# Performance work log

Hardware: AMD Instinct MI355X
Metric: run time of the kernel (lower is better)

The kernel has to match this reference:

```python
import jax, jax.numpy as jnp
import numpy as np

DIM = 1024
HEADS = 8
DIM_HEAD = 64
DIM_INNER = HEADS * DIM_HEAD  # 512


def setup_inputs() -> dict:
    key = jax.random.key(0)
    k1, k2, k3, k4 = jax.random.split(key, 4)
    x = jax.random.normal(k1, (1, 4096, DIM), dtype=jnp.float32)
    gamma = jnp.ones((DIM,), dtype=jnp.float32)
    w_qkv = jax.random.normal(k2, (DIM, 3 * DIM_INNER), dtype=jnp.float32) * (DIM ** -0.5)
    w_out = jax.random.normal(k3, (DIM_INNER, DIM), dtype=jnp.float32) * (DIM_INNER ** -0.5)
    return {"x": x, "gamma": gamma, "w_qkv": w_qkv, "w_out": w_out}


def _rmsnorm(x, gamma):
    # F.normalize(x, dim=-1) * sqrt(dim) * gamma
    norm = jnp.sqrt(jnp.sum(x * x, axis=-1, keepdims=True))
    x = x / jnp.maximum(norm, 1e-12)
    return x * (DIM ** 0.5) * gamma


def reference(x, gamma, w_qkv, w_out):
    b, n, _ = x.shape
    h, d = HEADS, DIM_HEAD
    normed = _rmsnorm(x, gamma)
    qkv = normed @ w_qkv  # [b, n, 3*h*d]
    qkv = qkv.reshape(b, n, 3, h, d)
    q = jnp.transpose(qkv[:, :, 0], (0, 2, 1, 3))  # b h n d
    k = jnp.transpose(qkv[:, :, 1], (0, 2, 1, 3))
    v = jnp.transpose(qkv[:, :, 2], (0, 2, 1, 3))
    # default_attention (faithful: scales q by d**0.5 as in source)
    q = q * (d ** 0.5)
    sim = jnp.einsum('bhid,bhjd->bhij', q, k)
    mask_value = -jnp.finfo(sim.dtype).max
    causal_mask = jnp.triu(jnp.ones((n, n), dtype=bool), 1)
    sim = jnp.where(causal_mask, mask_value, sim)
    attn = jax.nn.softmax(sim, axis=-1)
    out = jnp.einsum('bhij,bhjd->bhid', attn, v)  # b h n d
    out = jnp.transpose(out, (0, 2, 1, 3)).reshape(b, n, h * d)
    return out @ w_out  # [b, n, dim]
```

## Files before the change

kernel.cpp:

```cpp
#include <hip/hip_runtime.h>
#include <math.h>

#define SEQ 4096
#define DIM 1024
#define HEADS 8
#define DINNER 512
#define QKVW 1536
#define PAD 80

typedef unsigned short u16;
typedef __attribute__((ext_vector_type(8))) short s8v;
typedef __attribute__((ext_vector_type(4))) float f4v;
#define MFMA(a, b, c) __builtin_amdgcn_mfma_f32_16x16x32_bf16(a, b, c, 0, 0, 0)

__device__ __forceinline__ u16 f2bf(float f) {
    unsigned u = __float_as_uint(f);
    u += 0x7fff + ((u >> 16) & 1);
    return (u16)(u >> 16);
}
__device__ __forceinline__ float bf2f(u16 b) { return __uint_as_float(((unsigned)b) << 16); }

__global__ __launch_bounds__(256) void rmsnorm_split(const float* __restrict__ x,
                                                     const float* __restrict__ gamma,
                                                     u16* __restrict__ hi,
                                                     u16* __restrict__ lo) {
    __shared__ float red[4];
    const int row = blockIdx.x, t = threadIdx.x;
    const float* xr = x + (size_t)row * DIM;
    float v[4];
    float ss = 0.f;
#pragma unroll
    for (int i = 0; i < 4; ++i) { v[i] = xr[t + i * 256]; ss += v[i] * v[i]; }
#pragma unroll
    for (int off = 32; off >= 1; off >>= 1) ss += __shfl_xor(ss, off, 64);
    if ((t & 63) == 0) red[t >> 6] = ss;
    __syncthreads();
    float scale = 32.0f / fmaxf(sqrtf(red[0] + red[1] + red[2] + red[3]), 1e-12f);
#pragma unroll
    for (int i = 0; i < 4; ++i) {
        int c = t + i * 256;
        float y = v[i] * scale * gamma[c];
        u16 h = f2bf(y);
        hi[(size_t)row * DIM + c] = h;
        lo[(size_t)row * DIM + c] = f2bf(y - bf2f(h));
    }
}

__global__ __launch_bounds__(256) void transpose_split(const float* __restrict__ in,
                                                       u16* __restrict__ hi,
                                                       u16* __restrict__ lo,
                                                       int R, int C, int want_lo) {
    __shared__ float tile[64][65];
    const int c0 = blockIdx.x * 64, r0 = blockIdx.y * 64;
    const int t = threadIdx.x, col = t & 63, rb = t >> 6;
#pragma unroll
    for (int j = 0; j < 16; ++j)
        tile[rb + j * 4][col] = in[(size_t)(r0 + rb + j * 4) * C + c0 + col];
    __syncthreads();
#pragma unroll
    for (int j = 0; j < 16; ++j) {
        int cc = rb + j * 4;
        float v = tile[col][cc];
        size_t oi = (size_t)(c0 + cc) * R + r0 + col;
        u16 h = f2bf(v);
        hi[oi] = h;
        if (want_lo) lo[oi] = f2bf(v - bf2f(h));
    }
}

__global__ __launch_bounds__(256) void gemm_qkv_split(
    const u16* __restrict__ Ah, const u16* __restrict__ Al,
    const u16* __restrict__ Bh, const u16* __restrict__ Bl,
    u16* __restrict__ qh, u16* __restrict__ ql,
    u16* __restrict__ kh, u16* __restrict__ kl, u16* __restrict__ vtp) {
    __shared__ u16 Ash[64 * PAD], Asl[64 * PAD], Bsh[64 * PAD], Bsl[64 * PAD];
    const int t = threadIdx.x;
    const int bn = blockIdx.x * 64, bm = blockIdx.y * 64;
    const int w = t >> 6, lane = t & 63, m = lane & 15, q = lane >> 4;
    f4v acc[4] = {{0.f, 0.f, 0.f, 0.f}, {0.f, 0.f, 0.f, 0.f},
                  {0.f, 0.f, 0.f, 0.f}, {0.f, 0.f, 0.f, 0.f}};
    for (int k0 = 0; k0 < DIM; k0 += 64) {
        __syncthreads();
#pragma unroll
        for (int i = 0; i < 2; ++i) {
            int c = t + i * 256, row = c >> 3, ch = (c & 7) * 8;
            *(uint4*)&Ash[row * PAD + ch] = *(const uint4*)&Ah[(size_t)(bm + row) * DIM + k0 + ch];
            *(uint4*)&Asl[row * PAD + ch] = *(const uint4*)&Al[(size_t)(bm + row) * DIM + k0 + ch];
            *(uint4*)&Bsh[row * PAD + ch] = *(const uint4*)&Bh[(size_t)(bn + row) * DIM + k0 + ch];
            *(uint4*)&Bsl[row * PAD + ch] = *(const uint4*)&Bl[(size_t)(bn + row) * DIM + k0 + ch];
        }
        __syncthreads();
#pragma unroll
        for (int kk = 0; kk < 64; kk += 32) {
            s8v ah = *(const s8v*)&Ash[(w * 16 + m) * PAD + kk + q * 8];
            s8v al = *(const s8v*)&Asl[(w * 16 + m) * PAD + kk + q * 8];
#pragma unroll
            for (int ct = 0; ct < 4; ++ct) {
                s8v bh = *(const s8v*)&Bsh[(ct * 16 + m) * PAD + kk + q * 8];
                s8v bl = *(const s8v*)&Bsl[(ct * 16 + m) * PAD + kk + q * 8];
                acc[ct] = MFMA(ah, bh, acc[ct]);
                acc[ct] = MFMA(al, bh, acc[ct]);
                acc[ct] = MFMA(ah, bl, acc[ct]);
            }
        }
    }
    const int region = bn >> 9;
#pragma unroll
    for (int ct = 0; ct < 4; ++ct) {
#pragma unroll
        for (int r = 0; r < 4; ++r) {
            int gr = bm + w * 16 + q * 4 + r;
            int gc = bn + ct * 16 + m;
            float v = acc[ct][r];
            if (region == 0) {
                v *= 8.0f;
                u16 h = f2bf(v);
                qh[(size_t)gr * DINNER + gc] = h;
                ql[(size_t)gr * DINNER + gc] = f2bf(v - bf2f(h));
            } else if (region == 1) {
                u16 h = f2bf(v);
                kh[(size_t)gr * DINNER + (gc - 512)] = h;
                kl[(size_t)gr * DINNER + (gc - 512)] = f2bf(v - bf2f(h));
            } else {
                vtp[(size_t)(gc - 1024) * SEQ + gr] = f2bf(v);
            }
        }
    }
}

__global__ __launch_bounds__(256) void attn_mfma(
    const u16* __restrict__ qh, const u16* __restrict__ ql,
    const u16* __restrict__ kh, const u16* __restrict__ kl,
    const u16* __restrict__ vt, u16* __restrict__ atto) {
    __shared__ u16 Qh[64 * PAD], Ql[64 * PAD], KP[64 * PAD], Kl[64 * PAD], Vt[64 * PAD];
    const int t = threadIdx.x;
    const int qt = blockIdx.x, h = blockIdx.y;
    const int w = t >> 6, lane = t & 63, m = lane & 15, q = lane >> 4;

#pragma unroll
    for (int i = 0; i < 2; ++i) {
        int c = t + i * 256, row = c >> 3, ch = (c & 7) * 8;
        *(uint4*)&Qh[row * PAD + ch] =
            *(const uint4*)&qh[(size_t)(qt * 64 + row) * DINNER + h * 64 + ch];
        *(uint4*)&Ql[row * PAD + ch] =
            *(const uint4*)&ql[(size_t)(qt * 64 + row) * DINNER + h * 64 + ch];
    }

    f4v o[4] = {{0.f, 0.f, 0.f, 0.f}, {0.f, 0.f, 0.f, 0.f},
                {0.f, 0.f, 0.f, 0.f}, {0.f, 0.f, 0.f, 0.f}};
    float mi[4] = {-1e30f, -1e30f, -1e30f, -1e30f};
    float li[4] = {0.f, 0.f, 0.f, 0.f};

    for (int kt = 0; kt <= qt; ++kt) {
        __syncthreads();
#pragma unroll
        for (int i = 0; i < 2; ++i) {
            int c = t + i * 256, row = c >> 3, ch = (c & 7) * 8;
            *(uint4*)&KP[row * PAD + ch] =
                *(const uint4*)&kh[(size_t)(kt * 64 + row) * DINNER + h * 64 + ch];
            *(uint4*)&Kl[row * PAD + ch] =
                *(const uint4*)&kl[(size_t)(kt * 64 + row) * DINNER + h * 64 + ch];
            *(uint4*)&Vt[row * PAD + ch] =
                *(const uint4*)&vt[(size_t)(h * 64 + row) * SEQ + kt * 64 + ch];
        }
        __syncthreads();

        f4v s[4] = {{0.f, 0.f, 0.f, 0.f}, {0.f, 0.f, 0.f, 0.f},
                    {0.f, 0.f, 0.f, 0.f}, {0.f, 0.f, 0.f, 0.f}};
#pragma unroll
        for (int kk = 0; kk < 64; kk += 32) {
            s8v ah = *(const s8v*)&Qh[(w * 16 + m) * PAD + kk + q * 8];
            s8v al = *(const s8v*)&Ql[(w * 16 + m) * PAD + kk + q * 8];
#pragma unroll
            for (int ct = 0; ct < 4; ++ct) {
                s8v bh = *(const s8v*)&KP[(ct * 16 + m) * PAD + kk + q * 8];
                s8v bl = *(const s8v*)&Kl[(ct * 16 + m) * PAD + kk + q * 8];
                s[ct] = MFMA(ah, bh, s[ct]);
                s[ct] = MFMA(al, bh, s[ct]);
                s[ct] = MFMA(ah, bl, s[ct]);
            }
        }
        if (kt == qt) {
#pragma unroll
            for (int ct = 0; ct < 4; ++ct)
#pragma unroll
                for (int r = 0; r < 4; ++r)
                    if (ct * 16 + m > w * 16 + q * 4 + r) s[ct][r] = -1e30f;
        }

        float alpha[4];
#pragma unroll
        for (int r = 0; r < 4; ++r) {
            float rm = fmaxf(fmaxf(s[0][r], s[1][r]), fmaxf(s[2][r], s[3][r]));
#pragma unroll
            for (int off = 8; off >= 1; off >>= 1) rm = fmaxf(rm, __shfl_xor(rm, off, 64));
            float mn = fmaxf(mi[r], rm);
            alpha[r] = __expf(mi[r] - mn);
            mi[r] = mn;
            float rs = 0.f;
#pragma unroll
            for (int ct = 0; ct < 4; ++ct) {
                s[ct][r] = __expf(s[ct][r] - mn);
                rs += s[ct][r];
            }
#pragma unroll
            for (int off = 8; off >= 1; off >>= 1) rs += __shfl_xor(rs, off, 64);
            li[r] = li[r] * alpha[r] + rs;
        }

        __syncthreads();
#pragma unroll
        for (int ct = 0; ct < 4; ++ct)
#pragma unroll
            for (int r = 0; r < 4; ++r) {
                KP[(w * 16 + q * 4 + r) * PAD + ct * 16 + m] = f2bf(s[ct][r]);
                o[ct][r] *= alpha[r];
            }
#pragma unroll
        for (int kk = 0; kk < 64; kk += 32) {
            s8v ap = *(const s8v*)&KP[(w * 16 + m) * PAD + kk + q * 8];
#pragma unroll
            for (int ct = 0; ct < 4; ++ct) {
                s8v bv = *(const s8v*)&Vt[(ct * 16 + m) * PAD + kk + q * 8];
                o[ct] = MFMA(ap, bv, o[ct]);
            }
        }
    }

#pragma unroll
    for (int r = 0; r < 4; ++r) {
        float inv = 1.0f / li[r];
#pragma unroll
        for (int ct = 0; ct < 4; ++ct)
            atto[(size_t)(qt * 64 + w * 16 + q * 4 + r) * DINNER + h * 64 + ct * 16 + m] =
                f2bf(o[ct][r] * inv);
    }
}

__global__ __launch_bounds__(256) void gemm_out_bf16(const u16* __restrict__ A,
                                                     const u16* __restrict__ Bt,
                                                     float* __restrict__ C) {
    __shared__ u16 As[64 * PAD], Bs[64 * PAD];
    const int t = threadIdx.x;
    const int bn = blockIdx.x * 64, bm = blockIdx.y * 64;
    const int w = t >> 6, lane = t & 63, m = lane & 15, q = lane >> 4;
    f4v acc[4] = {{0.f, 0.f, 0.f, 0.f}, {0.f, 0.f, 0.f, 0.f},
                  {0.f, 0.f, 0.f, 0.f}, {0.f, 0.f, 0.f, 0.f}};
    for (int k0 = 0; k0 < DINNER; k0 += 64) {
        __syncthreads();
#pragma unroll
        for (int i = 0; i < 2; ++i) {
            int c = t + i * 256, row = c >> 3, ch = (c & 7) * 8;
            *(uint4*)&As[row * PAD + ch] = *(const uint4*)&A[(size_t)(bm + row) * DINNER + k0 + ch];
            *(uint4*)&Bs[row * PAD + ch] = *(const uint4*)&Bt[(size_t)(bn + row) * DINNER + k0 + ch];
        }
        __syncthreads();
#pragma unroll
        for (int kk = 0; kk < 64; kk += 32) {
            s8v a = *(const s8v*)&As[(w * 16 + m) * PAD + kk + q * 8];
#pragma unroll
            for (int ct = 0; ct < 4; ++ct) {
                s8v b = *(const s8v*)&Bs[(ct * 16 + m) * PAD + kk + q * 8];
                acc[ct] = MFMA(a, b, acc[ct]);
            }
        }
    }
#pragma unroll
    for (int ct = 0; ct < 4; ++ct)
#pragma unroll
        for (int r = 0; r < 4; ++r)
            C[(size_t)(bm + w * 16 + q * 4 + r) * DIM + bn + ct * 16 + m] = acc[ct][r];
}

extern "C" void kernel_launch(void* const* d_in, const int* in_sizes, int n_in,
                              void* d_out, int out_size, void* d_ws, size_t ws_size,
                              hipStream_t stream) {
    const float* x     = (const float*)d_in[0];
    const float* gamma = (const float*)d_in[1];
    const float* w_qkv = (const float*)d_in[2];
    const float* w_out = (const float*)d_in[3];
    float* out = (float*)d_out;

    u16* nh = (u16*)d_out;
    u16* nl = nh + (size_t)SEQ * DIM;

    u16* p = (u16*)d_ws;
    u16* wqt_h = p; p += (size_t)QKVW * DIM;
    u16* wqt_l = p; p += (size_t)QKVW * DIM;
    u16* wot   = p; p += (size_t)DIM * DINNER;
    u16* qh = p; p += (size_t)SEQ * DINNER;
    u16* ql = p; p += (size_t)SEQ * DINNER;
    u16* kh = p; p += (size_t)SEQ * DINNER;
    u16* kl = p; p += (size_t)SEQ * DINNER;
    u16* vt = p; p += (size_t)DINNER * SEQ;
    u16* atto = p; p += (size_t)SEQ * DINNER;

    transpose_split<<<dim3(QKVW / 64, DIM / 64), 256, 0, stream>>>(w_qkv, wqt_h, wqt_l,
                                                                   DIM, QKVW, 1);
    transpose_split<<<dim3(DIM / 64, DINNER / 64), 256, 0, stream>>>(w_out, wot, nullptr,
                                                                     DINNER, DIM, 0);
    rmsnorm_split<<<SEQ, 256, 0, stream>>>(x, gamma, nh, nl);
    gemm_qkv_split<<<dim3(QKVW / 64, SEQ / 64), 256, 0, stream>>>(nh, nl, wqt_h, wqt_l,
                                                                  qh, ql, kh, kl, vt);
    attn_mfma<<<dim3(SEQ / 64, HEADS), 256, 0, stream>>>(qh, ql, kh, kl, vt, atto);
    gemm_out_bf16<<<dim3(DIM / 64, SEQ / 64), 256, 0, stream>>>(atto, wot, out);
}
```

Before: 299.3 us.

## Split causal attention across key chunks with a separate merge kernel

Replaces the single per-query-tile attention kernel with a split-KV version. The keys are divided into chunks of 16 tiles, each block produces partial outputs plus per-row max and sum, and a merge kernel combines them into the attention output. The split kernel also loads Q straight into registers and prefetches the next K/V tile in registers. The goal is to fix the poor load balance and low parallelism of causal attention, where long query rows ran serially. In exchange it adds partial-output traffic (reusing the output buffer and workspace), an extra launch and a merge pass, and it falls back to the old kernel if the workspace is too small.

```diff
diff --git a/kernel.cpp b/kernel.cpp
--- a/kernel.cpp
+++ b/kernel.cpp
@@ -7,6 +7,7 @@
 #define DINNER 512
 #define QKVW 1536
 #define PAD 80
+#define CHUNK 16
 
 typedef unsigned short u16;
 typedef __attribute__((ext_vector_type(8))) short s8v;
@@ -128,6 +129,171 @@
     }
 }
 
+__global__ __launch_bounds__(256, 4) void attn_chunk(
+    const u16* __restrict__ qhp, const u16* __restrict__ qlp,
+    const u16* __restrict__ kh, const u16* __restrict__ kl,
+    const u16* __restrict__ vt,
+    float* __restrict__ po0, float* __restrict__ po1,
+    float* __restrict__ po2, float* __restrict__ po3,
+    float* __restrict__ ml) {
+    __shared__ u16 KP[64 * PAD], Kl[64 * PAD], Vt[64 * PAD];
+    const int t = threadIdx.x;
+    const int bx = blockIdx.x;
+    const int qt = 63 - (bx >> 2), c = bx & 3, h = blockIdx.y;
+    if (c * CHUNK > qt) return;
+    const int kt0 = c * CHUNK;
+    const int kt1 = (qt < kt0 + CHUNK - 1) ? qt : (kt0 + CHUNK - 1);
+    const int w = t >> 6, lane = t & 63, m = lane & 15, q = lane >> 4;
+
+    const size_t qrow = (size_t)(qt * 64 + w * 16 + m) * DINNER + h * 64;
+    const s8v qf_h0 = *(const s8v*)&qhp[qrow + q * 8];
+    const s8v qf_h1 = *(const s8v*)&qhp[qrow + 32 + q * 8];
+    const s8v qf_l0 = *(const s8v*)&qlp[qrow + q * 8];
+    const s8v qf_l1 = *(const s8v*)&qlp[qrow + 32 + q * 8];
+
+    f4v o[4] = {{0.f, 0.f, 0.f, 0.f}, {0.f, 0.f, 0.f, 0.f},
+                {0.f, 0.f, 0.f, 0.f}, {0.f, 0.f, 0.f, 0.f}};
+    float mi[4] = {-1e30f, -1e30f, -1e30f, -1e30f};
+    float li[4] = {0.f, 0.f, 0.f, 0.f};
+
+    uint4 rk[2], rl[2], rv[2];
+#pragma unroll
+    for (int i = 0; i < 2; ++i) {
+        int c2 = t + i * 256, row = c2 >> 3, ch = (c2 & 7) * 8;
+        rk[i] = *(const uint4*)&kh[(size_t)(kt0 * 64 + row) * DINNER + h * 64 + ch];
+        rl[i] = *(const uint4*)&kl[(size_t)(kt0 * 64 + row) * DINNER + h * 64 + ch];
+        rv[i] = *(const uint4*)&vt[(size_t)(h * 64 + row) * SEQ + kt0 * 64 + ch];
+    }
+
+    for (int kt = kt0; kt <= kt1; ++kt) {
+        __syncthreads();
+#pragma unroll
+        for (int i = 0; i < 2; ++i) {
+            int c2 = t + i * 256, row = c2 >> 3, ch = (c2 & 7) * 8;
+            *(uint4*)&KP[row * PAD + ch] = rk[i];
+            *(uint4*)&Kl[row * PAD + ch] = rl[i];
+            *(uint4*)&Vt[row * PAD + ch] = rv[i];
+        }
+        if (kt < kt1) {
+#pragma unroll
+            for (int i = 0; i < 2; ++i) {
+                int c2 = t + i * 256, row = c2 >> 3, ch = (c2 & 7) * 8;
+                rk[i] = *(const uint4*)&kh[(size_t)((kt + 1) * 64 + row) * DINNER + h * 64 + ch];
+                rl[i] = *(const uint4*)&kl[(size_t)((kt + 1) * 64 + row) * DINNER + h * 64 + ch];
+                rv[i] = *(const uint4*)&vt[(size_t)(h * 64 + row) * SEQ + (kt + 1) * 64 + ch];
+            }
+        }
+        __syncthreads();
+
+        f4v s[4] = {{0.f, 0.f, 0.f, 0.f}, {0.f, 0.f, 0.f, 0.f},
+                    {0.f, 0.f, 0.f, 0.f}, {0.f, 0.f, 0.f, 0.f}};
+#pragma unroll
+        for (int ct = 0; ct < 4; ++ct) {
+            s8v bh0 = *(const s8v*)&KP[(ct * 16 + m) * PAD + q * 8];
+            s8v bl0 = *(const s8v*)&Kl[(ct * 16 + m) * PAD + q * 8];
+            s[ct] = MFMA(qf_h0, bh0, s[ct]);
+            s[ct] = MFMA(qf_l0, bh0, s[ct]);
+            s[ct] = MFMA(qf_h0, bl0, s[ct]);
+            s8v bh1 = *(const s8v*)&KP[(ct * 16 + m) * PAD + 32 + q * 8];
+            s8v bl1 = *(const s8v*)&Kl[(ct * 16 + m) * PAD + 32 + q * 8];
+            s[ct] = MFMA(qf_h1, bh1, s[ct]);
+            s[ct] = MFMA(qf_l1, bh1, s[ct]);
+            s[ct] = MFMA(qf_h1, bl1, s[ct]);
+        }
+        if (kt == qt) {
+#pragma unroll
+            for (int ct = 0; ct < 4; ++ct)
+#pragma unroll
+                for (int r = 0; r < 4; ++r)
+                    if (ct * 16 + m > w * 16 + q * 4 + r) s[ct][r] = -1e30f;
+        }
+
+        float alpha[4];
+#pragma unroll
+        for (int r = 0; r < 4; ++r) {
+            float rm = fmaxf(fmaxf(s[0][r], s[1][r]), fmaxf(s[2][r], s[3][r]));
+#pragma unroll
+            for (int off = 8; off >= 1; off >>= 1) rm = fmaxf(rm, __shfl_xor(rm, off, 64));
+            float mn = fmaxf(mi[r], rm);
+            alpha[r] = __expf(mi[r] - mn);
+            mi[r] = mn;
+            float rs = 0.f;
+#pragma unroll
+            for (int ct = 0; ct < 4; ++ct) {
+                s[ct][r] = __expf(s[ct][r] - mn);
+                rs += s[ct][r];
+            }
+#pragma unroll
+            for (int off = 8; off >= 1; off >>= 1) rs += __shfl_xor(rs, off, 64);
+            li[r] = li[r] * alpha[r] + rs;
+        }
+
+        __syncthreads();
+#pragma unroll
+        for (int ct = 0; ct < 4; ++ct)
+#pragma unroll
+            for (int r = 0; r < 4; ++r) {
+                KP[(w * 16 + q * 4 + r) * PAD + ct * 16 + m] = f2bf(s[ct][r]);
+                o[ct][r] *= alpha[r];
+            }
+#pragma unroll
+        for (int kk = 0; kk < 64; kk += 32) {
+            s8v ap = *(const s8v*)&KP[(w * 16 + m) * PAD + kk + q * 8];
+#pragma unroll
+            for (int ct = 0; ct < 4; ++ct) {
+                s8v bv = *(const s8v*)&Vt[(ct * 16 + m) * PAD + kk + q * 8];
+                o[ct] = MFMA(ap, bv, o[ct]);
+            }
+        }
+    }
+
+    float* po = (c == 0) ? po0 : (c == 1) ? po1 : (c == 2) ? po2 : po3;
+    const size_t pbase = (size_t)(h * 64 + qt) * 64 * 64;
+#pragma unroll
+    for (int ct = 0; ct < 4; ++ct)
+#pragma unroll
+        for (int r = 0; r < 4; ++r)
+            po[pbase + (size_t)(w * 16 + q * 4 + r) * 64 + ct * 16 + m] = o[ct][r];
+    if (m == 0) {
+#pragma unroll
+        for (int r = 0; r < 4; ++r) {
+            int row = w * 16 + q * 4 + r;
+            ml[((size_t)(h * 64 + qt) * 4 + c) * 128 + row] = mi[r];
+            ml[((size_t)(h * 64 + qt) * 4 + c) * 128 + 64 + row] = li[r];
+        }
+    }
+}
+
+__global__ __launch_bounds__(256) void attn_merge(
+    const float* __restrict__ po0, const float* __restrict__ po1,
+    const float* __restrict__ po2, const float* __restrict__ po3,
+    const float* __restrict__ ml, u16* __restrict__ atto) {
+    const int qt = blockIdx.x, h = blockIdx.y;
+    const int nc = qt / CHUNK + 1;
+    const int t = threadIdx.x, col = t & 63, rg = t >> 6;
+    const size_t mlb = (size_t)(h * 64 + qt) * 4;
+    const size_t pb = (size_t)(h * 64 + qt) * 64;
+    for (int j = 0; j < 16; ++j) {
+        int row = rg * 16 + j;
+        float mv[4], lv[4];
+        float M = -1e30f;
+#pragma unroll
+        for (int cc = 0; cc < 4; ++cc)
+            if (cc < nc) {
+                mv[cc] = ml[(mlb + cc) * 128 + row];
+                lv[cc] = ml[(mlb + cc) * 128 + 64 + row];
+                M = fmaxf(M, mv[cc]);
+            }
+        const size_t oidx = (pb + row) * 64 + col;
+        float acc = 0.f, den = 0.f;
+        { float wg = __expf(mv[0] - M); den += lv[0] * wg; acc += wg * po0[oidx]; }
+        if (1 < nc) { float wg = __expf(mv[1] - M); den += lv[1] * wg; acc += wg * po1[oidx]; }
+        if (2 < nc) { float wg = __expf(mv[2] - M); den += lv[2] * wg; acc += wg * po2[oidx]; }
+        if (3 < nc) { float wg = __expf(mv[3] - M); den += lv[3] * wg; acc += wg * po3[oidx]; }
+        atto[(size_t)(qt * 64 + row) * DINNER + h * 64 + col] = f2bf(acc / den);
+    }
+}
+
 __global__ __launch_bounds__(256) void attn_mfma(
     const u16* __restrict__ qh, const u16* __restrict__ ql,
     const u16* __restrict__ kh, const u16* __restrict__ kl,
@@ -295,6 +461,13 @@
     u16* vt = p; p += (size_t)DINNER * SEQ;
     u16* atto = p; p += (size_t)SEQ * DINNER;
 
+    const size_t po_elems = (size_t)HEADS * 64 * 64 * 64;
+    float* po2 = (float*)p;
+    float* po3 = po2 + po_elems;
+    float* ml  = po3 + po_elems;
+    const size_t need = (size_t)((char*)(ml + (size_t)HEADS * 64 * 4 * 128) - (char*)d_ws);
+    const bool split = ws_size >= need;
+
     transpose_split<<<dim3(QKVW / 64, DIM / 64), 256, 0, stream>>>(w_qkv, wqt_h, wqt_l,
                                                                    DIM, QKVW, 1);
     transpose_split<<<dim3(DIM / 64, DINNER / 64), 256, 0, stream>>>(w_out, wot, nullptr,
@@ -302,6 +475,14 @@
     rmsnorm_split<<<SEQ, 256, 0, stream>>>(x, gamma, nh, nl);
     gemm_qkv_split<<<dim3(QKVW / 64, SEQ / 64), 256, 0, stream>>>(nh, nl, wqt_h, wqt_l,
                                                                   qh, ql, kh, kl, vt);
-    attn_mfma<<<dim3(SEQ / 64, HEADS), 256, 0, stream>>>(qh, ql, kh, kl, vt, atto);
+    if (split) {
+        float* po0 = (float*)d_out;
+        float* po1 = po0 + po_elems;
+        attn_chunk<<<dim3(256, HEADS), 256, 0, stream>>>(qh, ql, kh, kl, vt,
+                                                         po0, po1, po2, po3, ml);
+        attn_merge<<<dim3(SEQ / 64, HEADS), 256, 0, stream>>>(po0, po1, po2, po3, ml, atto);
+    } else {
+        attn_mfma<<<dim3(SEQ / 64, HEADS), 256, 0, stream>>>(qh, ql, kh, kl, vt, atto);
+    }
     gemm_out_bf16<<<dim3(DIM / 64, SEQ / 64), 256, 0, stream>>>(atto, wot, out);
 }
```

Result: slower. 411.1 us (+37.4%).
